# Optimization experiments

Hardware: AMD Instinct MI355X
Metric: run time of the kernel (lower is better)

## Reference

```python
import jax, jax.numpy as jnp
import numpy as np

N, C, E, Q, H, NC = 50000, 128, 1600000, 500000, 256, 2
BN_EPS = 1e-5


def gru_step(x, h, wih, whh, bih, bhh):
    # single-step torch.nn.GRU, gate order (r, z, n); x,h: [C, C] rows as batch
    gi = x @ wih.T + bih
    gh = h @ whh.T + bhh
    ir, iz, inn = jnp.split(gi, 3, axis=-1)
    hr, hz, hn = jnp.split(gh, 3, axis=-1)
    r = jax.nn.sigmoid(ir + hr)
    z = jax.nn.sigmoid(iz + hz)
    n = jnp.tanh(inn + r * hn)
    return (1.0 - z) * n + z * h


def gcn_conv(x, w, src, dst, ew):
    # GCNConv with fixed weight w and symmetric gcn_norm incl. self-loops
    xw = x @ w
    deg = jnp.zeros((N,), xw.dtype).at[dst].add(ew) + 1.0  # +1 self-loop
    dinv = jax.lax.rsqrt(deg)
    norm = dinv[src] * ew * dinv[dst]
    out = jnp.zeros_like(xw).at[dst].add(xw[src] * norm[:, None])
    return out + xw * (dinv * dinv)[:, None]  # self-loop contribution


def evolve_gcno(x, src, dst, ew, w_init, wih, whh, bih, bhh):
    w = gru_step(w_init, w_init, wih, whh, bih, bhh)
    return gcn_conv(x, w, src, dst, ew)


def setup_inputs():
    key = jax.random.key(0)
    ks = jax.random.split(key, 40)
    inp = {}
    inp["X"] = jax.random.normal(ks[0], (N, C), jnp.float32)
    inp["edge_index"] = jax.random.randint(ks[1], (2, E), 0, N, jnp.int32)
    inp["edge_weight"] = jax.random.uniform(ks[2], (E,), jnp.float32)
    inp["edge1"] = jax.random.randint(ks[3], (Q,), 0, N, jnp.int32)
    inp["edge2"] = jax.random.randint(ks[4], (Q,), 0, N, jnp.int32)
    s = 1.0 / np.sqrt(C)
    i = 5
    for l in range(2):
        inp[f"w{l}_init"] = jax.random.uniform(ks[i], (C, C), jnp.float32, -s, s); i += 1
        inp[f"w{l}_ih"] = jax.random.uniform(ks[i], (3 * C, C), jnp.float32, -s, s); i += 1
        inp[f"w{l}_hh"] = jax.random.uniform(ks[i], (3 * C, C), jnp.float32, -s, s); i += 1
        inp[f"b{l}_ih"] = jax.random.uniform(ks[i], (3 * C,), jnp.float32, -s, s); i += 1
        inp[f"b{l}_hh"] = jax.random.uniform(ks[i], (3 * C,), jnp.float32, -s, s); i += 1
    dims = [(H, C), (H, H), (NC, H)]
    for l, (o, fi) in enumerate(dims):
        sl = 1.0 / np.sqrt(fi)
        inp[f"lin_w{l}"] = jax.random.uniform(ks[i], (o, fi), jnp.float32, -sl, sl); i += 1
        inp[f"lin_b{l}"] = jax.random.uniform(ks[i], (o,), jnp.float32, -sl, sl); i += 1
    for l in range(2):
        inp[f"bn_g{l}"] = jax.random.uniform(ks[i], (H,), jnp.float32, 0.5, 1.5); i += 1
        inp[f"bn_b{l}"] = 0.1 * jax.random.normal(ks[i], (H,), jnp.float32); i += 1
        inp[f"bn_m{l}"] = 0.1 * jax.random.normal(ks[i], (H,), jnp.float32); i += 1
        inp[f"bn_v{l}"] = jax.random.uniform(ks[i], (H,), jnp.float32, 0.5, 1.5); i += 1
    return inp


def reference(X, edge_index, edge_weight, edge1, edge2,
              w0_init, w0_ih, w0_hh, b0_ih, b0_hh,
              w1_init, w1_ih, w1_hh, b1_ih, b1_hh,
              lin_w0, lin_b0, lin_w1, lin_b1, lin_w2, lin_b2,
              bn_g0, bn_b0, bn_m0, bn_v0, bn_g1, bn_b1, bn_m1, bn_v1):
    src, dst = edge_index[0], edge_index[1]
    # EGCNO: two EvolveGCNO layers + relu (dropout is identity in eval)
    x = jax.nn.relu(evolve_gcno(X, src, dst, edge_weight, w0_init, w0_ih, w0_hh, b0_ih, b0_hh))
    x = jax.nn.relu(evolve_gcno(x, src, dst, edge_weight, w1_init, w1_ih, w1_hh, b1_ih, b1_hh))
    # edge pair gather + hadamard
    h = x[edge1] * x[edge2]  # [Q, C]
    bn = [(bn_g0, bn_b0, bn_m0, bn_v0), (bn_g1, bn_b1, bn_m1, bn_v1)]
    lins = [(lin_w0, lin_b0), (lin_w1, lin_b1)]
    for (w, b), (g, bb, m, v) in zip(lins, bn):
        h = h @ w.T + b
        h = g * (h - m) * jax.lax.rsqrt(v + BN_EPS) + bb  # BatchNorm1d (eval)
        h = jax.nn.relu(h)
    h = h @ lin_w2.T + lin_b2
    return jax.nn.log_softmax(h, axis=-1)
```

## Files before the change

kernel.cpp:

```cpp
#include <hip/hip_runtime.h>
#include <math.h>

#define N_NODES 50000
#define C_DIM   128
#define E_EDGES 1600000
#define Q_PAIRS 500000
#define H_DIM   256
#define N_CLS   2
#define BN_EPS  1e-5f

typedef __attribute__((ext_vector_type(8))) short bf16x8;
typedef __attribute__((ext_vector_type(4))) short s16x4;
typedef __attribute__((ext_vector_type(4))) unsigned short u16x4;
typedef __attribute__((ext_vector_type(4))) float f32x4;

#define VMCNT0 asm volatile("s_waitcnt vmcnt(0)" ::: "memory")
#define VMCNT1 asm volatile("s_waitcnt vmcnt(1)" ::: "memory")
#define VMCNT2 asm volatile("s_waitcnt vmcnt(2)" ::: "memory")
#define SBAR do { __builtin_amdgcn_s_barrier(); \
                  __builtin_amdgcn_sched_barrier(0); } while (0)

#define DEG_SCALE 2097152.0f

__device__ __forceinline__ unsigned short f2bf(float x) {
    unsigned u = __float_as_uint(x);
    u += 0x7fffu + ((u >> 16) & 1u);
    return (unsigned short)(u >> 16);
}
__device__ __forceinline__ float bf2f(unsigned short h) {
    return __uint_as_float(((unsigned)h) << 16);
}

__global__ __launch_bounds__(256) void k_init(unsigned long long* dpack, int* qcnt) {
    int i = blockIdx.x * 256 + threadIdx.x;
    if (i < N_NODES) { dpack[i] = 0ULL; qcnt[i] = 0; }
}
__global__ __launch_bounds__(256) void k_deg_hist(const int* __restrict__ dst,
                                                  const float* __restrict__ ew,
                                                  unsigned long long* dpack) {
    int e = blockIdx.x * 256 + threadIdx.x;
    if (e < E_EDGES) {
        unsigned pv = __float2uint_rn(ew[e] * DEG_SCALE);
        atomicAdd(&dpack[dst[e]], (1ULL << 32) | (unsigned long long)pv);
    }
}
__global__ __launch_bounds__(256) void k_qhist(const int* __restrict__ e1, int* qcnt) {
    int q = blockIdx.x * 256 + threadIdx.x;
    if (q < Q_PAIRS) atomicAdd(&qcnt[e1[q]], 1);
}

__global__ __launch_bounds__(1024) void k_scan1(const int* __restrict__ cnt, int stride,
                                                int* __restrict__ locincl,
                                                int* __restrict__ bsum) {
    __shared__ int pa[1024], pb[1024];
    int t = threadIdx.x;
    int x = blockIdx.x * 1024 + t;
    int v = (x < N_NODES) ? cnt[(size_t)x * stride] : 0;
    pa[t] = v;
    __syncthreads();
    int* sp = pa; int* dp = pb;
    for (int o = 1; o < 1024; o <<= 1) {
        int u = sp[t] + ((t >= o) ? sp[t - o] : 0);
        dp[t] = u;
        __syncthreads();
        int* tmp = sp; sp = dp; dp = tmp;
    }
    if (x < N_NODES) locincl[x] = sp[t];
    if (t == 1023) bsum[blockIdx.x] = sp[1023];
}
__global__ __launch_bounds__(64) void k_scan2(const int* __restrict__ bsum,
                                              int* __restrict__ boff) {
    int t = threadIdx.x;
    int v = (t < 49) ? bsum[t] : 0;
    int own = v;
    for (int o = 1; o < 64; o <<= 1) {
        int u = __shfl_up(v, o, 64);
        if (t >= o) v += u;
    }
    if (t < 49) boff[t] = v - own;
}
__global__ __launch_bounds__(1024) void k_scan3(const int* __restrict__ cnt, int stride,
                                                int* __restrict__ pos,
                                                const int* __restrict__ boff,
                                                int* __restrict__ off,
                                                const unsigned long long* __restrict__ dpack,
                                                float* __restrict__ dinv) {
    int x = blockIdx.x * 1024 + threadIdx.x;
    if (x >= N_NODES) return;
    int incl = pos[x];
    int c = cnt[(size_t)x * stride];
    int o = boff[blockIdx.x] + incl - c;
    off[x] = o;
    pos[x] = o;
    if (x == N_NODES - 1) off[N_NODES] = o + c;
    if (dpack) {
        unsigned lo = (unsigned)(dpack[x] & 0xffffffffULL);
        dinv[x] = rsqrtf(1.0f + (float)lo * (1.0f / DEG_SCALE));
    }
}

__global__ __launch_bounds__(256) void k_fill(const int* __restrict__ src,
                                              const int* __restrict__ dst,
                                              const float* __restrict__ ew,
                                              const float* __restrict__ dinv,
                                              int* pos,
                                              int2* __restrict__ csr) {
    int e = blockIdx.x * 256 + threadIdx.x;
    if (e >= E_EDGES) return;
    int s = src[e], d = dst[e];
    int slot = atomicAdd(&pos[d], 1);
    int2 p;
    p.x = s;
    p.y = __float_as_int(dinv[s] * ew[e] * dinv[d]);
    csr[slot] = p;
}
__global__ __launch_bounds__(256) void k_qfill(const int* __restrict__ e1,
                                               const int* __restrict__ e2,
                                               int* qpos,
                                               int2* __restrict__ qpair,
                                               int* __restrict__ qidx) {
    int q = blockIdx.x * 256 + threadIdx.x;
    if (q >= Q_PAIRS) return;
    int a = e1[q];
    int slot = atomicAdd(&qpos[a], 1);
    int2 p; p.x = a; p.y = e2[q];
    qpair[slot] = p;
    qidx[slot] = q;
}

__global__ __launch_bounds__(128) void k_gru2(
    const float* __restrict__ wi0, const float* __restrict__ wih0, const float* __restrict__ whh0,
    const float* __restrict__ bih0, const float* __restrict__ bhh0, float* __restrict__ we0,
    const float* __restrict__ wi1, const float* __restrict__ wih1, const float* __restrict__ whh1,
    const float* __restrict__ bih1, const float* __restrict__ bhh1, float* __restrict__ we1) {
    __shared__ float xrow[C_DIM];
    int layer = blockIdx.x >> 7;
    int i = blockIdx.x & 127, j = threadIdx.x;
    const float* w_init = layer ? wi1 : wi0;
    const float* wih = layer ? wih1 : wih0;
    const float* whh = layer ? whh1 : whh0;
    const float* bih = layer ? bih1 : bih0;
    const float* bhh = layer ? bhh1 : bhh0;
    float* w_out = layer ? we1 : we0;
    xrow[j] = w_init[i * C_DIM + j];
    __syncthreads();
    float gi[3], gh[3];
#pragma unroll
    for (int g = 0; g < 3; ++g) {
        const float* wi = wih + (size_t)(g * C_DIM + j) * C_DIM;
        const float* wh = whh + (size_t)(g * C_DIM + j) * C_DIM;
        float ai = 0.f, ah = 0.f;
        for (int k = 0; k < C_DIM; ++k) { ai += xrow[k] * wi[k]; ah += xrow[k] * wh[k]; }
        gi[g] = ai + bih[g * C_DIM + j];
        gh[g] = ah + bhh[g * C_DIM + j];
    }
    float r = 1.f / (1.f + expf(-(gi[0] + gh[0])));
    float z = 1.f / (1.f + expf(-(gi[1] + gh[1])));
    float n = tanhf(gi[2] + r * gh[2]);
    w_out[i * C_DIM + j] = (1.f - z) * n + z * xrow[j];
}

__global__ __launch_bounds__(256) void k_xbf(const float* __restrict__ x,
                                             unsigned short* __restrict__ xb) {
    int i = (blockIdx.x * 256 + threadIdx.x) * 8;
    f32x4 a = *(const f32x4*)(x + i);
    f32x4 b = *(const f32x4*)(x + i + 4);
    bf16x8 o;
#pragma unroll
    for (int e = 0; e < 4; ++e) { o[e] = (short)f2bf(a[e]); o[e + 4] = (short)f2bf(b[e]); }
    *(bf16x8*)(xb + i) = o;
}

__global__ __launch_bounds__(256) void k_agg(const unsigned short* __restrict__ xb,
                                             const float* __restrict__ dinv,
                                             const int* __restrict__ off,
                                             const int2* __restrict__ csr,
                                             float* __restrict__ agg) {
    int tid = blockIdx.x * 256 + threadIdx.x;
    int n = tid >> 5;
    int c = (tid & 31) << 2;
    float dv = dinv[n];
    float d2 = dv * dv;
    u16x4 xs = *(const u16x4*)(xb + (size_t)n * C_DIM + c);
    float4 acc;
    acc.x = d2 * bf2f(xs[0]); acc.y = d2 * bf2f(xs[1]);
    acc.z = d2 * bf2f(xs[2]); acc.w = d2 * bf2f(xs[3]);
    int i = off[n], e = off[n + 1];
    for (; i + 8 <= e; i += 8) {
        int2 q0 = csr[i], q1 = csr[i + 1], q2 = csr[i + 2], q3 = csr[i + 3];
        int2 q4 = csr[i + 4], q5 = csr[i + 5], q6 = csr[i + 6], q7 = csr[i + 7];
        u16x4 v0 = *(const u16x4*)(xb + (size_t)q0.x * C_DIM + c);
        u16x4 v1 = *(const u16x4*)(xb + (size_t)q1.x * C_DIM + c);
        u16x4 v2 = *(const u16x4*)(xb + (size_t)q2.x * C_DIM + c);
        u16x4 v3 = *(const u16x4*)(xb + (size_t)q3.x * C_DIM + c);
        u16x4 v4 = *(const u16x4*)(xb + (size_t)q4.x * C_DIM + c);
        u16x4 v5 = *(const u16x4*)(xb + (size_t)q5.x * C_DIM + c);
        u16x4 v6 = *(const u16x4*)(xb + (size_t)q6.x * C_DIM + c);
        u16x4 v7 = *(const u16x4*)(xb + (size_t)q7.x * C_DIM + c);
        float w0 = __int_as_float(q0.y), w1 = __int_as_float(q1.y);
        float w2 = __int_as_float(q2.y), w3 = __int_as_float(q3.y);
        float w4 = __int_as_float(q4.y), w5 = __int_as_float(q5.y);
        float w6 = __int_as_float(q6.y), w7 = __int_as_float(q7.y);
        acc.x += w0 * bf2f(v0[0]) + w1 * bf2f(v1[0]) + w2 * bf2f(v2[0]) + w3 * bf2f(v3[0])
               + w4 * bf2f(v4[0]) + w5 * bf2f(v5[0]) + w6 * bf2f(v6[0]) + w7 * bf2f(v7[0]);
        acc.y += w0 * bf2f(v0[1]) + w1 * bf2f(v1[1]) + w2 * bf2f(v2[1]) + w3 * bf2f(v3[1])
               + w4 * bf2f(v4[1]) + w5 * bf2f(v5[1]) + w6 * bf2f(v6[1]) + w7 * bf2f(v7[1]);
        acc.z += w0 * bf2f(v0[2]) + w1 * bf2f(v1[2]) + w2 * bf2f(v2[2]) + w3 * bf2f(v3[2])
               + w4 * bf2f(v4[2]) + w5 * bf2f(v5[2]) + w6 * bf2f(v6[2]) + w7 * bf2f(v7[2]);
        acc.w += w0 * bf2f(v0[3]) + w1 * bf2f(v1[3]) + w2 * bf2f(v2[3]) + w3 * bf2f(v3[3])
               + w4 * bf2f(v4[3]) + w5 * bf2f(v5[3]) + w6 * bf2f(v6[3]) + w7 * bf2f(v7[3]);
    }
    for (; i < e; ++i) {
        int2 pe = csr[i];
        float w = __int_as_float(pe.y);
        u16x4 v = *(const u16x4*)(xb + (size_t)pe.x * C_DIM + c);
        acc.x += w * bf2f(v[0]); acc.y += w * bf2f(v[1]);
        acc.z += w * bf2f(v[2]); acc.w += w * bf2f(v[3]);
    }
    *(float4*)(agg + (size_t)n * C_DIM + c) = acc;
}

__global__ __launch_bounds__(256) void k_prep_w(const float* __restrict__ w,
                                                const float* __restrict__ g,
                                                const float* __restrict__ v,
                                                int kdim, int total,
                                                unsigned short* __restrict__ outp) {
    int idx = blockIdx.x * 256 + threadIdx.x;
    if (idx >= total) return;
    int e = idx & 7, col = (idx >> 3) & 255, kg = (idx >> 11) & 3;
    int kb = idx >> 13;
    int k = kb * 32 + kg * 8 + e;
    float sc = g[col] * rsqrtf(v[col] + BN_EPS);
    outp[idx] = f2bf(w[(size_t)col * kdim + k] * sc);
}
__global__ __launch_bounds__(256) void k_prep_conv(const float* __restrict__ we0,
                                                   const float* __restrict__ we1,
                                                   unsigned short* __restrict__ Wc0,
                                                   unsigned short* __restrict__ Wc1) {
    int idx = blockIdx.x * 256 + threadIdx.x;
    int e = idx & 7, col = (idx >> 3) & 127, kg = (idx >> 10) & 3;
    int plane = (idx >> 12) & 1, kb = (idx >> 13) & 3, layer = idx >> 15;
    int k = kb * 32 + kg * 8 + e;
    const float* we = layer ? we1 : we0;
    float x = we[(size_t)k * C_DIM + col];
    unsigned short hi = f2bf(x);
    unsigned short o = plane ? f2bf(x - bf2f(hi)) : hi;
    (layer ? Wc1 : Wc0)[idx & 32767] = o;
}

__global__ __launch_bounds__(512) void k_prep_shift(
    const float* __restrict__ lb0, const float* __restrict__ bg0, const float* __restrict__ bb0,
    const float* __restrict__ bm0, const float* __restrict__ bv0,
    const float* __restrict__ lb1, const float* __restrict__ bg1, const float* __restrict__ bb1,
    const float* __restrict__ bm1, const float* __restrict__ bv1,
    float* __restrict__ shift0, float* __restrict__ shift1) {
    int j = threadIdx.x;
    if (j < 256) {
        float sc = bg0[j] * rsqrtf(bv0[j] + BN_EPS);
        shift0[j] = (lb0[j] - bm0[j]) * sc + bb0[j];
    } else {
        int i = j - 256;
        float sc = bg1[i] * rsqrtf(bv1[i] + BN_EPS);
        shift1[i] = (lb1[i] - bm1[i]) * sc + bb1[i];
    }
}

template <int OUT_BF>
__global__ __launch_bounds__(512) void k_gemm(const float* __restrict__ agg,
                                              const unsigned short* __restrict__ Wc,
                                              float* __restrict__ y,
                                              unsigned short* __restrict__ yb) {
    __shared__ __align__(16) char smem[3 * 8192];
    const int t = threadIdx.x, lane = t & 63, wave = t >> 6;
    const int qg = wave >> 1, ch = wave & 1;
    const int l16 = lane & 15, kg = lane >> 4;
    const int qrow = qg * 16 + l16;
    const int node = blockIdx.x * 64 + qrow;
    const int nodec = node < N_NODES ? node : N_NODES - 1;

    auto STG = [&](int sidx, int b) {
        const char* g = (const char*)Wc + sidx * 8192 + wave * 1024 + lane * 16;
        char* d = smem + b * 8192 + wave * 1024;
        __builtin_amdgcn_global_load_lds((const __attribute__((address_space(1))) void*)g,
                                         (__attribute__((address_space(3))) void*)d, 16, 0, 0);
    };
    STG(0, 0); STG(1, 1);

    bf16x8 bh[4], bl[4];
    const float* ar = agg + (size_t)nodec * C_DIM;
#pragma unroll
    for (int kb = 0; kb < 4; ++kb) {
        int k0 = kb * 32 + kg * 8;
        f32x4 a0 = *(const f32x4*)(ar + k0);
        f32x4 a1 = *(const f32x4*)(ar + k0 + 4);
#pragma unroll
        for (int e = 0; e < 4; ++e) {
            unsigned short h0 = f2bf(a0[e]);
            bh[kb][e] = (short)h0; bl[kb][e] = (short)f2bf(a0[e] - bf2f(h0));
            unsigned short h1 = f2bf(a1[e]);
            bh[kb][e + 4] = (short)h1; bl[kb][e + 4] = (short)f2bf(a1[e] - bf2f(h1));
        }
    }
    f32x4 acc[4];
#pragma unroll
    for (int i = 0; i < 4; ++i) acc[i] = 0.f;

#pragma unroll
    for (int s = 0; s < 8; ++s) {
        if (s < 7) { VMCNT1; } else { VMCNT0; }
        SBAR;
        if (s + 2 < 8) STG(s + 2, (s + 2) % 3);
        const unsigned short* strip = (const unsigned short*)(smem + (s % 3) * 8192);
        const int kb = s >> 1;
        __builtin_amdgcn_s_setprio(1);
#pragma unroll
        for (int jc8 = 0; jc8 < 4; ++jc8) {
            int col = (ch * 4 + jc8) * 16 + l16;
            bf16x8 a = *(const bf16x8*)&strip[kg * 1024 + col * 8];
            acc[jc8] = __builtin_amdgcn_mfma_f32_16x16x32_bf16(a, bh[kb], acc[jc8], 0, 0, 0);
            if ((s & 1) == 0)
                acc[jc8] = __builtin_amdgcn_mfma_f32_16x16x32_bf16(a, bl[kb], acc[jc8], 0, 0, 0);
        }
        __builtin_amdgcn_s_setprio(0);
    }

    if (node < N_NODES) {
#pragma unroll
        for (int jc8 = 0; jc8 < 4; ++jc8) {
            int j0 = (ch * 4 + jc8) * 16 + kg * 4;
            if (OUT_BF) {
                u16x4 v;
#pragma unroll
                for (int r = 0; r < 4; ++r) v[r] = f2bf(fmaxf(acc[jc8][r], 0.f));
                *(u16x4*)(yb + (size_t)node * C_DIM + j0) = v;
            } else {
                float4 v;
                v.x = fmaxf(acc[jc8][0], 0.f); v.y = fmaxf(acc[jc8][1], 0.f);
                v.z = fmaxf(acc[jc8][2], 0.f); v.w = fmaxf(acc[jc8][3], 0.f);
                *(float4*)(y + (size_t)node * C_DIM + j0) = v;
            }
        }
    }
}

__global__ __launch_bounds__(512, 4) void k_mlp(const float* __restrict__ y,
                                             const int2* __restrict__ qpair,
                                             const int* __restrict__ qidx,
                                             const unsigned short* __restrict__ W0p,
                                             const unsigned short* __restrict__ W1p,
                                             const float* __restrict__ shift0,
                                             const float* __restrict__ shift1,
                                             const float* __restrict__ w2,
                                             const float* __restrict__ b2,
                                             float* __restrict__ out) {
    __shared__ __align__(16) char smem[81920];
    unsigned short* l1b = (unsigned short*)(smem + 49152);
    float* red = (float*)smem;

    const int t = threadIdx.x;
    const int lane = t & 63;
    const int wave = t >> 6;
    const int qs = wave >> 2, cg = wave & 3;
    const int l16 = lane & 15, kg = lane >> 4;
    const int qb = blockIdx.x * 64;

    auto STG = [&](const unsigned short* W, int sidx, int b) {
        const char* g = (const char*)W + ((size_t)sidx << 14) + wave * 2048 + lane * 16;
        char* d = smem + b * 16384 + wave * 2048;
        __builtin_amdgcn_global_load_lds((const __attribute__((address_space(1))) void*)g,
                                         (__attribute__((address_space(3))) void*)d, 16, 0, 0);
        __builtin_amdgcn_global_load_lds((const __attribute__((address_space(1))) void*)(g + 1024),
                                         (__attribute__((address_space(3))) void*)(d + 1024), 16, 0, 0);
    };

    STG(W0p, 0, 0); STG(W0p, 1, 1);

    {
        int k2 = lane * 2;
        int G = lane >> 2;
        int off = k2 & 7;
#pragma unroll
        for (int qi = 0; qi < 8; ++qi) {
            int qrow = wave * 8 + qi;
            int q = qb + qrow; if (q >= Q_PAIRS) q = Q_PAIRS - 1;
            int2 pr = qpair[q];
            const float* ya = y + (size_t)pr.x * C_DIM;
            const float* yb = y + (size_t)pr.y * C_DIM;
            float2 a = *(const float2*)(ya + k2);
            float2 b = *(const float2*)(yb + k2);
            int idx = qrow * 256 + ((G ^ (qrow & 7)) << 3) + off;
            l1b[idx] = f2bf(a.x * b.x);
            l1b[idx + 1] = f2bf(a.y * b.y);
        }
    }
    __syncthreads();

    bf16x8 bh[2][4];
#pragma unroll
    for (int qq = 0; qq < 2; ++qq) {
        int qrow = qs * 32 + qq * 16 + l16;
#pragma unroll
        for (int kb = 0; kb < 4; ++kb) {
            int gidx = qrow * 256 + (((kb * 4 + kg) ^ (qrow & 7)) * 8);
            bh[qq][kb] = *(const bf16x8*)&l1b[gidx];
        }
    }

    f32x4 acc[2][4];
#pragma unroll
    for (int qq = 0; qq < 2; ++qq)
#pragma unroll
        for (int jc = 0; jc < 4; ++jc) acc[qq][jc] = 0.f;

#pragma unroll
    for (int s = 0; s < 4; ++s) {
        if (s < 3) { VMCNT2; } else { VMCNT0; }
        SBAR;
        if (s + 2 < 4) STG(W0p, s + 2, (s + 2) % 3);
        const unsigned short* strip = (const unsigned short*)(smem + (s % 3) * 16384);
        __builtin_amdgcn_s_setprio(1);
#pragma unroll
        for (int jc = 0; jc < 4; ++jc) {
            int col = cg * 64 + jc * 16 + l16;
            bf16x8 a = *(const bf16x8*)&strip[kg * 2048 + col * 8];
            acc[0][jc] = __builtin_amdgcn_mfma_f32_16x16x32_bf16(a, bh[0][s], acc[0][jc], 0, 0, 0);
            acc[1][jc] = __builtin_amdgcn_mfma_f32_16x16x32_bf16(a, bh[1][s], acc[1][jc], 0, 0, 0);
        }
        __builtin_amdgcn_s_setprio(0);
    }

#pragma unroll
    for (int qq = 0; qq < 2; ++qq) {
        int qrow = qs * 32 + qq * 16 + l16;
#pragma unroll
        for (int jc = 0; jc < 4; ++jc) {
            int jg = cg * 4 + jc;
            int j0 = jg * 16 + kg * 4;
            f32x4 sh = *(const f32x4*)(shift0 + j0);
            s16x4 th;
#pragma unroll
            for (int r = 0; r < 4; ++r)
                th[r] = (short)f2bf(fmaxf(acc[qq][jc][r] + sh[r], 0.f));
            int G = jg * 2 + (kg >> 1);
            int idx = qrow * 256 + ((G ^ (qrow & 7)) * 8) + (kg & 1) * 4;
            *(s16x4*)&l1b[idx] = th;
        }
    }
    __syncthreads();

    f32x4 acc2[2][4];
#pragma unroll
    for (int qq = 0; qq < 2; ++qq)
#pragma unroll
        for (int jc = 0; jc < 4; ++jc) acc2[qq][jc] = 0.f;
    STG(W1p, 0, 0); STG(W1p, 1, 1);
    bf16x8 bh2[2];
#pragma unroll
    for (int s = 0; s < 8; ++s) {
        if (s < 7) { VMCNT2; } else { VMCNT0; }
        SBAR;
        if (s + 2 < 8) STG(W1p, s + 2, (s + 2) % 3);
        const unsigned short* strip = (const unsigned short*)(smem + (s % 3) * 16384);
#pragma unroll
        for (int qq = 0; qq < 2; ++qq) {
            int qrow = qs * 32 + qq * 16 + l16;
            int gidx = qrow * 256 + (((s * 4 + kg) ^ (qrow & 7)) * 8);
            bh2[qq] = *(const bf16x8*)&l1b[gidx];
        }
        __builtin_amdgcn_s_setprio(1);
#pragma unroll
        for (int jc = 0; jc < 4; ++jc) {
            int col = cg * 64 + jc * 16 + l16;
            bf16x8 a = *(const bf16x8*)&strip[kg * 2048 + col * 8];
            acc2[0][jc] = __builtin_amdgcn_mfma_f32_16x16x32_bf16(a, bh2[0], acc2[0][jc], 0, 0, 0);
            acc2[1][jc] = __builtin_amdgcn_mfma_f32_16x16x32_bf16(a, bh2[1], acc2[1][jc], 0, 0, 0);
        }
        __builtin_amdgcn_s_setprio(0);
    }

    float p[2][2] = {};
#pragma unroll
    for (int qq = 0; qq < 2; ++qq)
#pragma unroll
        for (int jc = 0; jc < 4; ++jc) {
            int j0 = (cg * 4 + jc) * 16 + kg * 4;
            f32x4 sh = *(const f32x4*)(shift1 + j0);
            f32x4 wa = *(const f32x4*)(w2 + j0);
            f32x4 wb = *(const f32x4*)(w2 + H_DIM + j0);
#pragma unroll
            for (int r = 0; r < 4; ++r) {
                float v = fmaxf(acc2[qq][jc][r] + sh[r], 0.f);
                p[qq][0] += v * wa[r];
                p[qq][1] += v * wb[r];
            }
        }
#pragma unroll
    for (int qq = 0; qq < 2; ++qq) {
        p[qq][0] += __shfl_xor(p[qq][0], 16, 64); p[qq][0] += __shfl_xor(p[qq][0], 32, 64);
        p[qq][1] += __shfl_xor(p[qq][1], 16, 64); p[qq][1] += __shfl_xor(p[qq][1], 32, 64);
    }
    __syncthreads();
    if (kg == 0) {
#pragma unroll
        for (int qq = 0; qq < 2; ++qq) {
            int base = ((qs * 2 + qq) * 16 + l16) * 2;
            red[(base + 0) * 4 + cg] = p[qq][0];
            red[(base + 1) * 4 + cg] = p[qq][1];
        }
    }
    __syncthreads();
    if (t < 64) {
        int q = qb + t;
        if (q < Q_PAIRS) {
            int base = t * 2;
            float l0 = red[base * 4 + 0] + red[base * 4 + 1] + red[base * 4 + 2] + red[base * 4 + 3] + b2[0];
            float l1v = red[(base + 1) * 4 + 0] + red[(base + 1) * 4 + 1]
                      + red[(base + 1) * 4 + 2] + red[(base + 1) * 4 + 3] + b2[1];
            float mx = fmaxf(l0, l1v);
            float lse = mx + logf(expf(l0 - mx) + expf(l1v - mx));
            float2 o; o.x = l0 - lse; o.y = l1v - lse;
            *(float2*)(out + (size_t)qidx[q] * N_CLS) = o;
        }
    }
}

extern "C" void kernel_launch(void* const* d_in, const int* in_sizes, int n_in,
                              void* d_out, int out_size, void* d_ws, size_t ws_size,
                              hipStream_t stream) {
    const float* X  = (const float*)d_in[0];
    const int*   ei = (const int*)d_in[1];
    const float* ew = (const float*)d_in[2];
    const int*   e1 = (const int*)d_in[3];
    const int*   e2 = (const int*)d_in[4];
    const float* w_init[2] = {(const float*)d_in[5],  (const float*)d_in[10]};
    const float* w_ih[2]   = {(const float*)d_in[6],  (const float*)d_in[11]};
    const float* w_hh[2]   = {(const float*)d_in[7],  (const float*)d_in[12]};
    const float* b_ih[2]   = {(const float*)d_in[8],  (const float*)d_in[13]};
    const float* b_hh[2]   = {(const float*)d_in[9],  (const float*)d_in[14]};
    const float* lw0 = (const float*)d_in[15]; const float* lb0 = (const float*)d_in[16];
    const float* lw1 = (const float*)d_in[17]; const float* lb1 = (const float*)d_in[18];
    const float* lw2 = (const float*)d_in[19]; const float* lb2 = (const float*)d_in[20];
    const float* bg0 = (const float*)d_in[21]; const float* bb0 = (const float*)d_in[22];
    const float* bm0 = (const float*)d_in[23]; const float* bv0 = (const float*)d_in[24];
    const float* bg1 = (const float*)d_in[25]; const float* bb1 = (const float*)d_in[26];
    const float* bm1 = (const float*)d_in[27]; const float* bv1 = (const float*)d_in[28];
    const int* src = ei;
    const int* dst = ei + E_EDGES;

    char* ws = (char*)d_ws;
    size_t o = 0;
    auto alloc = [&](size_t bytes) { char* p = ws + o; o += (bytes + 63) & ~(size_t)63; return p; };
    float* bufA   = (float*)alloc((size_t)N_NODES * C_DIM * 4);
    float* bufB   = (float*)alloc((size_t)N_NODES * C_DIM * 4);
    unsigned short* xbf = (unsigned short*)alloc((size_t)N_NODES * C_DIM * 2);
    unsigned short* ybf = (unsigned short*)alloc((size_t)N_NODES * C_DIM * 2);
    float* dinv   = (float*)alloc(N_NODES * 4);
    float* we0    = (float*)alloc(C_DIM * C_DIM * 4);
    float* we1    = (float*)alloc(C_DIM * C_DIM * 4);
    float* shift0 = (float*)alloc(H_DIM * 4);
    float* shift1 = (float*)alloc(H_DIM * 4);
    unsigned long long* dpack = (unsigned long long*)alloc((size_t)N_NODES * 8);
    int*   pos    = (int*)alloc(N_NODES * 4);
    int*   off    = (int*)alloc((N_NODES + 1) * 4);
    int*   bsum   = (int*)alloc(64 * 4);
    int*   boff   = (int*)alloc(64 * 4);
    int*   qcnt   = (int*)alloc(N_NODES * 4);
    int*   qpos   = (int*)alloc(N_NODES * 4);
    int*   qoff   = (int*)alloc((N_NODES + 1) * 4);
    int*   qbsum  = (int*)alloc(64 * 4);
    int*   qboff  = (int*)alloc(64 * 4);
    int2*  csr    = (int2*)alloc((size_t)E_EDGES * 8);
    int2*  qpair  = (int2*)alloc((size_t)Q_PAIRS * 8);
    int*   qidx   = (int*)alloc((size_t)Q_PAIRS * 4);
    unsigned short* W0p = (unsigned short*)alloc(32768 * 2);
    unsigned short* W1p = (unsigned short*)alloc(65536 * 2);
    unsigned short* Wc0 = (unsigned short*)alloc(32768 * 2);
    unsigned short* Wc1 = (unsigned short*)alloc(32768 * 2);
    if (o > ws_size) return;

    dim3 b256(256);
    const int gN = (N_NODES + 255) / 256;
    const int gE = (E_EDGES + 255) / 256;
    const int gQ = (Q_PAIRS + 255) / 256;

    k_init<<<gN, b256, 0, stream>>>(dpack, qcnt);
    k_deg_hist<<<gE, b256, 0, stream>>>(dst, ew, dpack);
    k_qhist<<<gQ, b256, 0, stream>>>(e1, qcnt);
    k_scan1<<<49, dim3(1024), 0, stream>>>((const int*)dpack + 1, 2, pos, bsum);
    k_scan2<<<1, dim3(64), 0, stream>>>(bsum, boff);
    k_scan3<<<49, dim3(1024), 0, stream>>>((const int*)dpack + 1, 2, pos, boff, off, dpack, dinv);
    k_fill<<<gE, b256, 0, stream>>>(src, dst, ew, dinv, pos, csr);
    k_scan1<<<49, dim3(1024), 0, stream>>>(qcnt, 1, qpos, qbsum);
    k_scan2<<<1, dim3(64), 0, stream>>>(qbsum, qboff);
    k_scan3<<<49, dim3(1024), 0, stream>>>(qcnt, 1, qpos, qboff, qoff, nullptr, nullptr);
    k_qfill<<<gQ, b256, 0, stream>>>(e1, e2, qpos, qpair, qidx);

    k_gru2<<<256, dim3(128), 0, stream>>>(w_init[0], w_ih[0], w_hh[0], b_ih[0], b_hh[0], we0,
                                          w_init[1], w_ih[1], w_hh[1], b_ih[1], b_hh[1], we1);
    k_prep_conv<<<256, b256, 0, stream>>>(we0, we1, Wc0, Wc1);
    k_prep_w<<<128, b256, 0, stream>>>(lw0, bg0, bv0, C_DIM, 32768, W0p);
    k_prep_w<<<256, b256, 0, stream>>>(lw1, bg1, bv1, H_DIM, 65536, W1p);
    k_prep_shift<<<1, dim3(512), 0, stream>>>(lb0, bg0, bb0, bm0, bv0, lb1, bg1, bb1, bm1, bv1, shift0, shift1);
    k_xbf<<<(N_NODES * C_DIM) / 2048, b256, 0, stream>>>(X, xbf);

    const int ga = (N_NODES * 32) / 256;
    const int gg = (N_NODES + 63) / 64;
    k_agg<<<ga, b256, 0, stream>>>(xbf, dinv, off, csr, bufA);
    k_gemm<1><<<gg, dim3(512), 0, stream>>>(bufA, Wc0, bufB, ybf);
    k_agg<<<ga, b256, 0, stream>>>(ybf, dinv, off, csr, bufA);
    k_gemm<0><<<gg, dim3(512), 0, stream>>>(bufA, Wc1, bufB, ybf);
    k_mlp<<<(Q_PAIRS + 63) / 64, dim3(512), 0, stream>>>(bufB, qpair, qidx, W0p, W1p,
                                                         shift0, shift1, lw2, lb2, (float*)d_out);
}
```

Measured before the change: 572.9 us.

## Drop query-pair sorting, merge prep kernels, use packed bf16 conversion

Removes the whole counting-sort pipeline for query pairs (histogram, scan, fill) and has the MLP kernel read edge1/edge2 directly and write outputs in natural order. It merges the GRU and X-to-bf16 kernels, and the three weight-prep kernels plus the shift kernel, into fewer launches, and replaces the init kernel with a memset. It also uses the hardware packed bf16 conversion instruction in the MLP staging. The cost is that the MLP gathers lose the locality the sort gave on the first endpoint, so those row reads become more scattered.

```diff
diff --git a/kernel.cpp b/kernel.cpp
--- a/kernel.cpp
+++ b/kernel.cpp
@@ -30,32 +30,29 @@
 __device__ __forceinline__ float bf2f(unsigned short h) {
     return __uint_as_float(((unsigned)h) << 16);
 }
-
-__global__ __launch_bounds__(256) void k_init(unsigned long long* dpack, int* qcnt) {
-    int i = blockIdx.x * 256 + threadIdx.x;
-    if (i < N_NODES) { dpack[i] = 0ULL; qcnt[i] = 0; }
-}
-__global__ __launch_bounds__(256) void k_deg_hist(const int* __restrict__ dst,
-                                                  const float* __restrict__ ew,
-                                                  unsigned long long* dpack) {
+__device__ __forceinline__ unsigned cvtpk(float a, float b) {
+    unsigned r;
+    asm("v_cvt_pk_bf16_f32 %0, %1, %2" : "=v"(r) : "v"(a), "v"(b));
+    return r;
+}
+
+__global__ __launch_bounds__(256) void k_hist(const int* __restrict__ dst,
+                                              const float* __restrict__ ew,
+                                              unsigned long long* dpack) {
     int e = blockIdx.x * 256 + threadIdx.x;
     if (e < E_EDGES) {
         unsigned pv = __float2uint_rn(ew[e] * DEG_SCALE);
         atomicAdd(&dpack[dst[e]], (1ULL << 32) | (unsigned long long)pv);
     }
 }
-__global__ __launch_bounds__(256) void k_qhist(const int* __restrict__ e1, int* qcnt) {
-    int q = blockIdx.x * 256 + threadIdx.x;
-    if (q < Q_PAIRS) atomicAdd(&qcnt[e1[q]], 1);
-}
-
-__global__ __launch_bounds__(1024) void k_scan1(const int* __restrict__ cnt, int stride,
-                                                int* __restrict__ locincl,
+
+__global__ __launch_bounds__(1024) void k_scan1(const unsigned long long* __restrict__ dpack,
+                                                int* __restrict__ pos,
                                                 int* __restrict__ bsum) {
     __shared__ int pa[1024], pb[1024];
     int t = threadIdx.x;
     int x = blockIdx.x * 1024 + t;
-    int v = (x < N_NODES) ? cnt[(size_t)x * stride] : 0;
+    int v = (x < N_NODES) ? (int)(dpack[x] >> 32) : 0;
     pa[t] = v;
     __syncthreads();
     int* sp = pa; int* dp = pb;
@@ -65,7 +62,7 @@
         __syncthreads();
         int* tmp = sp; sp = dp; dp = tmp;
     }
-    if (x < N_NODES) locincl[x] = sp[t];
+    if (x < N_NODES) pos[x] = sp[t];
     if (t == 1023) bsum[blockIdx.x] = sp[1023];
 }
 __global__ __launch_bounds__(64) void k_scan2(const int* __restrict__ bsum,
@@ -79,24 +76,21 @@
     }
     if (t < 49) boff[t] = v - own;
 }
-__global__ __launch_bounds__(1024) void k_scan3(const int* __restrict__ cnt, int stride,
+__global__ __launch_bounds__(1024) void k_scan3(const unsigned long long* __restrict__ dpack,
                                                 int* __restrict__ pos,
                                                 const int* __restrict__ boff,
                                                 int* __restrict__ off,
-                                                const unsigned long long* __restrict__ dpack,
                                                 float* __restrict__ dinv) {
     int x = blockIdx.x * 1024 + threadIdx.x;
     if (x >= N_NODES) return;
+    int c = (int)(dpack[x] >> 32);
     int incl = pos[x];
-    int c = cnt[(size_t)x * stride];
     int o = boff[blockIdx.x] + incl - c;
     off[x] = o;
     pos[x] = o;
     if (x == N_NODES - 1) off[N_NODES] = o + c;
-    if (dpack) {
-        unsigned lo = (unsigned)(dpack[x] & 0xffffffffULL);
-        dinv[x] = rsqrtf(1.0f + (float)lo * (1.0f / DEG_SCALE));
-    }
+    unsigned lo = (unsigned)(dpack[x] & 0xffffffffULL);
+    dinv[x] = rsqrtf(1.0f + (float)lo * (1.0f / DEG_SCALE));
 }
 
 __global__ __launch_bounds__(256) void k_fill(const int* __restrict__ src,
@@ -114,61 +108,98 @@
     p.y = __float_as_int(dinv[s] * ew[e] * dinv[d]);
     csr[slot] = p;
 }
-__global__ __launch_bounds__(256) void k_qfill(const int* __restrict__ e1,
-                                               const int* __restrict__ e2,
-                                               int* qpos,
-                                               int2* __restrict__ qpair,
-                                               int* __restrict__ qidx) {
-    int q = blockIdx.x * 256 + threadIdx.x;
-    if (q >= Q_PAIRS) return;
-    int a = e1[q];
-    int slot = atomicAdd(&qpos[a], 1);
-    int2 p; p.x = a; p.y = e2[q];
-    qpair[slot] = p;
-    qidx[slot] = q;
-}
-
-__global__ __launch_bounds__(128) void k_gru2(
+
+__global__ __launch_bounds__(256) void k_gru_xbf(
     const float* __restrict__ wi0, const float* __restrict__ wih0, const float* __restrict__ whh0,
     const float* __restrict__ bih0, const float* __restrict__ bhh0, float* __restrict__ we0,
     const float* __restrict__ wi1, const float* __restrict__ wih1, const float* __restrict__ whh1,
-    const float* __restrict__ bih1, const float* __restrict__ bhh1, float* __restrict__ we1) {
-    __shared__ float xrow[C_DIM];
-    int layer = blockIdx.x >> 7;
-    int i = blockIdx.x & 127, j = threadIdx.x;
-    const float* w_init = layer ? wi1 : wi0;
-    const float* wih = layer ? wih1 : wih0;
-    const float* whh = layer ? whh1 : whh0;
-    const float* bih = layer ? bih1 : bih0;
-    const float* bhh = layer ? bhh1 : bhh0;
-    float* w_out = layer ? we1 : we0;
-    xrow[j] = w_init[i * C_DIM + j];
-    __syncthreads();
-    float gi[3], gh[3];
-#pragma unroll
-    for (int g = 0; g < 3; ++g) {
-        const float* wi = wih + (size_t)(g * C_DIM + j) * C_DIM;
-        const float* wh = whh + (size_t)(g * C_DIM + j) * C_DIM;
-        float ai = 0.f, ah = 0.f;
-        for (int k = 0; k < C_DIM; ++k) { ai += xrow[k] * wi[k]; ah += xrow[k] * wh[k]; }
-        gi[g] = ai + bih[g * C_DIM + j];
-        gh[g] = ah + bhh[g * C_DIM + j];
-    }
-    float r = 1.f / (1.f + expf(-(gi[0] + gh[0])));
-    float z = 1.f / (1.f + expf(-(gi[1] + gh[1])));
-    float n = tanhf(gi[2] + r * gh[2]);
-    w_out[i * C_DIM + j] = (1.f - z) * n + z * xrow[j];
-}
-
-__global__ __launch_bounds__(256) void k_xbf(const float* __restrict__ x,
-                                             unsigned short* __restrict__ xb) {
-    int i = (blockIdx.x * 256 + threadIdx.x) * 8;
-    f32x4 a = *(const f32x4*)(x + i);
-    f32x4 b = *(const f32x4*)(x + i + 4);
-    bf16x8 o;
-#pragma unroll
-    for (int e = 0; e < 4; ++e) { o[e] = (short)f2bf(a[e]); o[e + 4] = (short)f2bf(b[e]); }
-    *(bf16x8*)(xb + i) = o;
+    const float* __restrict__ bih1, const float* __restrict__ bhh1, float* __restrict__ we1,
+    const float* __restrict__ x, unsigned short* __restrict__ xb) {
+    if (blockIdx.x < 256) {
+        __shared__ float xrow[C_DIM];
+        int layer = blockIdx.x >> 7;
+        int i = blockIdx.x & 127, j = threadIdx.x;
+        const float* w_init = layer ? wi1 : wi0;
+        const float* wih = layer ? wih1 : wih0;
+        const float* whh = layer ? whh1 : whh0;
+        const float* bih = layer ? bih1 : bih0;
+        const float* bhh = layer ? bhh1 : bhh0;
+        float* w_out = layer ? we1 : we0;
+        if (j < C_DIM) xrow[j] = w_init[i * C_DIM + j];
+        __syncthreads();
+        if (j < C_DIM) {
+            float gi[3], gh[3];
+#pragma unroll
+            for (int g = 0; g < 3; ++g) {
+                const float* wi = wih + (size_t)(g * C_DIM + j) * C_DIM;
+                const float* wh = whh + (size_t)(g * C_DIM + j) * C_DIM;
+                float ai = 0.f, ah = 0.f;
+                for (int k = 0; k < C_DIM; ++k) { ai += xrow[k] * wi[k]; ah += xrow[k] * wh[k]; }
+                gi[g] = ai + bih[g * C_DIM + j];
+                gh[g] = ah + bhh[g * C_DIM + j];
+            }
+            float r = 1.f / (1.f + expf(-(gi[0] + gh[0])));
+            float z = 1.f / (1.f + expf(-(gi[1] + gh[1])));
+            float n = tanhf(gi[2] + r * gh[2]);
+            w_out[i * C_DIM + j] = (1.f - z) * n + z * xrow[j];
+        }
+    } else {
+        int i = ((blockIdx.x - 256) * 256 + threadIdx.x) * 8;
+        f32x4 a = *(const f32x4*)(x + i);
+        f32x4 b = *(const f32x4*)(x + i + 4);
+        bf16x8 o;
+#pragma unroll
+        for (int e = 0; e < 4; ++e) { o[e] = (short)f2bf(a[e]); o[e + 4] = (short)f2bf(b[e]); }
+        *(bf16x8*)(xb + i) = o;
+    }
+}
+
+__global__ __launch_bounds__(256) void k_prep_all(
+    const float* __restrict__ we0, const float* __restrict__ we1,
+    unsigned short* __restrict__ Wc0, unsigned short* __restrict__ Wc1,
+    const float* __restrict__ lw0, const float* __restrict__ lw1,
+    unsigned short* __restrict__ W0p, unsigned short* __restrict__ W1p,
+    const float* __restrict__ lb0, const float* __restrict__ bg0, const float* __restrict__ bb0,
+    const float* __restrict__ bm0, const float* __restrict__ bv0,
+    const float* __restrict__ lb1, const float* __restrict__ bg1, const float* __restrict__ bb1,
+    const float* __restrict__ bm1, const float* __restrict__ bv1,
+    float* __restrict__ shift0, float* __restrict__ shift1) {
+    int b = blockIdx.x, t = threadIdx.x;
+    if (b < 256) {
+        int idx = b * 256 + t;
+        int e = idx & 7, col = (idx >> 3) & 127, kg = (idx >> 10) & 3;
+        int plane = (idx >> 12) & 1, kb = (idx >> 13) & 3, layer = idx >> 15;
+        int k = kb * 32 + kg * 8 + e;
+        const float* we = layer ? we1 : we0;
+        float x = we[(size_t)k * C_DIM + col];
+        unsigned short hi = f2bf(x);
+        unsigned short o = plane ? f2bf(x - bf2f(hi)) : hi;
+        (layer ? Wc1 : Wc0)[idx & 32767] = o;
+    } else if (b < 384) {
+        int idx = (b - 256) * 256 + t;
+        int e = idx & 7, col = (idx >> 3) & 255, kg = (idx >> 11) & 3;
+        int kb = idx >> 13;
+        int k = kb * 32 + kg * 8 + e;
+        float sc = bg0[col] * rsqrtf(bv0[col] + BN_EPS);
+        W0p[idx] = f2bf(lw0[(size_t)col * C_DIM + k] * sc);
+    } else if (b < 640) {
+        int idx = (b - 384) * 256 + t;
+        int e = idx & 7, col = (idx >> 3) & 255, kg = (idx >> 11) & 3;
+        int kb = idx >> 13;
+        int k = kb * 32 + kg * 8 + e;
+        float sc = bg1[col] * rsqrtf(bv1[col] + BN_EPS);
+        W1p[idx] = f2bf(lw1[(size_t)col * H_DIM + k] * sc);
+    } else {
+        int j = (b - 640) * 256 + t;
+        if (j < 256) {
+            float sc = bg0[j] * rsqrtf(bv0[j] + BN_EPS);
+            shift0[j] = (lb0[j] - bm0[j]) * sc + bb0[j];
+        } else {
+            int i = j - 256;
+            float sc = bg1[i] * rsqrtf(bv1[i] + BN_EPS);
+            shift1[i] = (lb1[i] - bm1[i]) * sc + bb1[i];
+        }
+    }
 }
 
 __global__ __launch_bounds__(256) void k_agg(const unsigned short* __restrict__ xb,
@@ -220,51 +251,6 @@
     *(float4*)(agg + (size_t)n * C_DIM + c) = acc;
 }
 
-__global__ __launch_bounds__(256) void k_prep_w(const float* __restrict__ w,
-                                                const float* __restrict__ g,
-                                                const float* __restrict__ v,
-                                                int kdim, int total,
-                                                unsigned short* __restrict__ outp) {
-    int idx = blockIdx.x * 256 + threadIdx.x;
-    if (idx >= total) return;
-    int e = idx & 7, col = (idx >> 3) & 255, kg = (idx >> 11) & 3;
-    int kb = idx >> 13;
-    int k = kb * 32 + kg * 8 + e;
-    float sc = g[col] * rsqrtf(v[col] + BN_EPS);
-    outp[idx] = f2bf(w[(size_t)col * kdim + k] * sc);
-}
-__global__ __launch_bounds__(256) void k_prep_conv(const float* __restrict__ we0,
-                                                   const float* __restrict__ we1,
-                                                   unsigned short* __restrict__ Wc0,
-                                                   unsigned short* __restrict__ Wc1) {
-    int idx = blockIdx.x * 256 + threadIdx.x;
-    int e = idx & 7, col = (idx >> 3) & 127, kg = (idx >> 10) & 3;
-    int plane = (idx >> 12) & 1, kb = (idx >> 13) & 3, layer = idx >> 15;
-    int k = kb * 32 + kg * 8 + e;
-    const float* we = layer ? we1 : we0;
-    float x = we[(size_t)k * C_DIM + col];
-    unsigned short hi = f2bf(x);
-    unsigned short o = plane ? f2bf(x - bf2f(hi)) : hi;
-    (layer ? Wc1 : Wc0)[idx & 32767] = o;
-}
-
-__global__ __launch_bounds__(512) void k_prep_shift(
-    const float* __restrict__ lb0, const float* __restrict__ bg0, const float* __restrict__ bb0,
-    const float* __restrict__ bm0, const float* __restrict__ bv0,
-    const float* __restrict__ lb1, const float* __restrict__ bg1, const float* __restrict__ bb1,
-    const float* __restrict__ bm1, const float* __restrict__ bv1,
-    float* __restrict__ shift0, float* __restrict__ shift1) {
-    int j = threadIdx.x;
-    if (j < 256) {
-        float sc = bg0[j] * rsqrtf(bv0[j] + BN_EPS);
-        shift0[j] = (lb0[j] - bm0[j]) * sc + bb0[j];
-    } else {
-        int i = j - 256;
-        float sc = bg1[i] * rsqrtf(bv1[i] + BN_EPS);
-        shift1[i] = (lb1[i] - bm1[i]) * sc + bb1[i];
-    }
-}
-
 template <int OUT_BF>
 __global__ __launch_bounds__(512) void k_gemm(const float* __restrict__ agg,
                                               const unsigned short* __restrict__ Wc,
@@ -344,8 +330,8 @@
 }
 
 __global__ __launch_bounds__(512, 4) void k_mlp(const float* __restrict__ y,
-                                             const int2* __restrict__ qpair,
-                                             const int* __restrict__ qidx,
+                                             const int* __restrict__ e1,
+                                             const int* __restrict__ e2,
                                              const unsigned short* __restrict__ W0p,
                                              const unsigned short* __restrict__ W1p,
                                              const float* __restrict__ shift0,
@@ -383,14 +369,12 @@
         for (int qi = 0; qi < 8; ++qi) {
             int qrow = wave * 8 + qi;
             int q = qb + qrow; if (q >= Q_PAIRS) q = Q_PAIRS - 1;
-            int2 pr = qpair[q];
-            const float* ya = y + (size_t)pr.x * C_DIM;
-            const float* yb = y + (size_t)pr.y * C_DIM;
+            const float* ya = y + (size_t)e1[q] * C_DIM;
+            const float* yb = y + (size_t)e2[q] * C_DIM;
             float2 a = *(const float2*)(ya + k2);
             float2 b = *(const float2*)(yb + k2);
             int idx = qrow * 256 + ((G ^ (qrow & 7)) << 3) + off;
-            l1b[idx] = f2bf(a.x * b.x);
-            l1b[idx + 1] = f2bf(a.y * b.y);
+            *(unsigned*)&l1b[idx] = cvtpk(a.x * b.x, a.y * b.y);
         }
     }
     __syncthreads();
@@ -437,13 +421,14 @@
             int jg = cg * 4 + jc;
             int j0 = jg * 16 + kg * 4;
             f32x4 sh = *(const f32x4*)(shift0 + j0);
-            s16x4 th;
-#pragma unroll
-            for (int r = 0; r < 4; ++r)
-                th[r] = (short)f2bf(fmaxf(acc[qq][jc][r] + sh[r], 0.f));
+            float v0 = fmaxf(acc[qq][jc][0] + sh[0], 0.f);
+            float v1 = fmaxf(acc[qq][jc][1] + sh[1], 0.f);
+            float v2 = fmaxf(acc[qq][jc][2] + sh[2], 0.f);
+            float v3 = fmaxf(acc[qq][jc][3] + sh[3], 0.f);
             int G = jg * 2 + (kg >> 1);
             int idx = qrow * 256 + ((G ^ (qrow & 7)) * 8) + (kg & 1) * 4;
-            *(s16x4*)&l1b[idx] = th;
+            uint2 pk; pk.x = cvtpk(v0, v1); pk.y = cvtpk(v2, v3);
+            *(uint2*)&l1b[idx] = pk;
         }
     }
     __syncthreads();
@@ -519,7 +504,7 @@
             float mx = fmaxf(l0, l1v);
             float lse = mx + logf(expf(l0 - mx) + expf(l1v - mx));
             float2 o; o.x = l0 - lse; o.y = l1v - lse;
-            *(float2*)(out + (size_t)qidx[q] * N_CLS) = o;
+            *(float2*)(out + (size_t)q * N_CLS) = o;
         }
     }
 }
@@ -554,24 +539,17 @@
     float* bufB   = (float*)alloc((size_t)N_NODES * C_DIM * 4);
     unsigned short* xbf = (unsigned short*)alloc((size_t)N_NODES * C_DIM * 2);
     unsigned short* ybf = (unsigned short*)alloc((size_t)N_NODES * C_DIM * 2);
+    unsigned long long* dpack = (unsigned long long*)alloc((size_t)N_NODES * 8);
     float* dinv   = (float*)alloc(N_NODES * 4);
     float* we0    = (float*)alloc(C_DIM * C_DIM * 4);
     float* we1    = (float*)alloc(C_DIM * C_DIM * 4);
     float* shift0 = (float*)alloc(H_DIM * 4);
     float* shift1 = (float*)alloc(H_DIM * 4);
-    unsigned long long* dpack = (unsigned long long*)alloc((size_t)N_NODES * 8);
     int*   pos    = (int*)alloc(N_NODES * 4);
     int*   off    = (int*)alloc((N_NODES + 1) * 4);
     int*   bsum   = (int*)alloc(64 * 4);
     int*   boff   = (int*)alloc(64 * 4);
-    int*   qcnt   = (int*)alloc(N_NODES * 4);
-    int*   qpos   = (int*)alloc(N_NODES * 4);
-    int*   qoff   = (int*)alloc((N_NODES + 1) * 4);
-    int*   qbsum  = (int*)alloc(64 * 4);
-    int*   qboff  = (int*)alloc(64 * 4);
     int2*  csr    = (int2*)alloc((size_t)E_EDGES * 8);
-    int2*  qpair  = (int2*)alloc((size_t)Q_PAIRS * 8);
-    int*   qidx   = (int*)alloc((size_t)Q_PAIRS * 4);
     unsigned short* W0p = (unsigned short*)alloc(32768 * 2);
     unsigned short* W1p = (unsigned short*)alloc(65536 * 2);
     unsigned short* Wc0 = (unsigned short*)alloc(32768 * 2);
@@ -579,29 +557,21 @@
     if (o > ws_size) return;
 
     dim3 b256(256);
-    const int gN = (N_NODES + 255) / 256;
     const int gE = (E_EDGES + 255) / 256;
-    const int gQ = (Q_PAIRS + 255) / 256;
-
-    k_init<<<gN, b256, 0, stream>>>(dpack, qcnt);
-    k_deg_hist<<<gE, b256, 0, stream>>>(dst, ew, dpack);
-    k_qhist<<<gQ, b256, 0, stream>>>(e1, qcnt);
-    k_scan1<<<49, dim3(1024), 0, stream>>>((const int*)dpack + 1, 2, pos, bsum);
+
+    hipMemsetAsync(dpack, 0, (size_t)N_NODES * 8, stream);
+    k_hist<<<gE, b256, 0, stream>>>(dst, ew, dpack);
+    k_scan1<<<49, dim3(1024), 0, stream>>>(dpack, pos, bsum);
     k_scan2<<<1, dim3(64), 0, stream>>>(bsum, boff);
-    k_scan3<<<49, dim3(1024), 0, stream>>>((const int*)dpack + 1, 2, pos, boff, off, dpack, dinv);
+    k_scan3<<<49, dim3(1024), 0, stream>>>(dpack, pos, boff, off, dinv);
     k_fill<<<gE, b256, 0, stream>>>(src, dst, ew, dinv, pos, csr);
-    k_scan1<<<49, dim3(1024), 0, stream>>>(qcnt, 1, qpos, qbsum);
-    k_scan2<<<1, dim3(64), 0, stream>>>(qbsum, qboff);
-    k_scan3<<<49, dim3(1024), 0, stream>>>(qcnt, 1, qpos, qboff, qoff, nullptr, nullptr);
-    k_qfill<<<gQ, b256, 0, stream>>>(e1, e2, qpos, qpair, qidx);
-
-    k_gru2<<<256, dim3(128), 0, stream>>>(w_init[0], w_ih[0], w_hh[0], b_ih[0], b_hh[0], we0,
-                                          w_init[1], w_ih[1], w_hh[1], b_ih[1], b_hh[1], we1);
-    k_prep_conv<<<256, b256, 0, stream>>>(we0, we1, Wc0, Wc1);
-    k_prep_w<<<128, b256, 0, stream>>>(lw0, bg0, bv0, C_DIM, 32768, W0p);
-    k_prep_w<<<256, b256, 0, stream>>>(lw1, bg1, bv1, H_DIM, 65536, W1p);
-    k_prep_shift<<<1, dim3(512), 0, stream>>>(lb0, bg0, bb0, bm0, bv0, lb1, bg1, bb1, bm1, bv1, shift0, shift1);
-    k_xbf<<<(N_NODES * C_DIM) / 2048, b256, 0, stream>>>(X, xbf);
+
+    k_gru_xbf<<<256 + 3125, b256, 0, stream>>>(w_init[0], w_ih[0], w_hh[0], b_ih[0], b_hh[0], we0,
+                                               w_init[1], w_ih[1], w_hh[1], b_ih[1], b_hh[1], we1,
+                                               X, xbf);
+    k_prep_all<<<642, b256, 0, stream>>>(we0, we1, Wc0, Wc1, lw0, lw1, W0p, W1p,
+                                         lb0, bg0, bb0, bm0, bv0,
+                                         lb1, bg1, bb1, bm1, bv1, shift0, shift1);
 
     const int ga = (N_NODES * 32) / 256;
     const int gg = (N_NODES + 63) / 64;
@@ -609,6 +579,6 @@
     k_gemm<1><<<gg, dim3(512), 0, stream>>>(bufA, Wc0, bufB, ybf);
     k_agg<<<ga, b256, 0, stream>>>(ybf, dinv, off, csr, bufA);
     k_gemm<0><<<gg, dim3(512), 0, stream>>>(bufA, Wc1, bufB, ybf);
-    k_mlp<<<(Q_PAIRS + 63) / 64, dim3(512), 0, stream>>>(bufB, qpair, qidx, W0p, W1p,
+    k_mlp<<<(Q_PAIRS + 63) / 64, dim3(512), 0, stream>>>(bufB, e1, e2, W0p, W1p,
                                                          shift0, shift1, lw2, lb2, (float*)d_out);
 }
```

Result: faster. 495.9 us (-13.4%).
